# Optimization experiments

Measured on AMD Instinct MI355X. Metric: run time of the kernel, lower is better.

## Reference

```python
import jax, jax.numpy as jnp
import numpy as np

HALF_LOG_2PI = 0.5 * float(np.log(2.0 * np.pi))


def setup_inputs() -> dict:
    key = jax.random.key(0)
    k1, k2 = jax.random.split(key)
    N, D = 16384, 2048
    x = jax.random.normal(k1, (N, D), dtype=jnp.float32)
    raw_params = jax.random.normal(k2, (2 * D,), dtype=jnp.float32)
    # chain spanning tree: edges (i, i+1) for i in 0..D-2  -> shape [D-1, 2]
    idx = jnp.arange(D - 1, dtype=jnp.int64)
    edges = jnp.stack([idx, idx + 1], axis=1)
    return {"x": x, "raw_params": raw_params, "edges": edges}


def reference(x, raw_params, edges):
    # x: [N, D] float; raw_params: [2D] float; edges: [E, 2] int
    D = x.shape[1]
    means = jnp.tanh(raw_params[:D]) * 2.0               # [D]
    stds = jax.nn.softplus(raw_params[D:]) + 1e-6         # [D]
    # Each edge (i, j) contributes logN(x_i) + logN(x_j); equivalently each
    # feature k contributes deg(k) * logN(x_k), deg = endpoint multiplicity.
    deg = jnp.zeros((D,), dtype=x.dtype).at[edges.reshape(-1)].add(1.0)  # [D]
    z = (x - means) / stds                                # [N, D]
    logp = -0.5 * z * z - jnp.log(stds) - HALF_LOG_2PI    # [N, D]
    return logp @ deg                                     # [N]
```

## Files before the change

### kernel.cpp

```cpp
#include <hip/hip_runtime.h>
#include <math.h>

#define HALF_LOG_2PI_F 0.9189385332046727f

typedef float f32x4 __attribute__((ext_vector_type(4)));

__global__ void clt_prep_kernel(const float* __restrict__ rp,
                                const int* __restrict__ edges,
                                float* __restrict__ A,
                                float* __restrict__ B,
                                float* __restrict__ csum,
                                int D, int E) {
    extern __shared__ float sdeg[];
    for (int k = threadIdx.x; k < D; k += blockDim.x) sdeg[k] = 0.0f;
    __syncthreads();
    for (int e = threadIdx.x; e < E; e += blockDim.x) {
        atomicAdd(&sdeg[edges[2 * e]], 1.0f);
        atomicAdd(&sdeg[edges[2 * e + 1]], 1.0f);
    }
    __syncthreads();
    float local_c = 0.0f;
    for (int k = threadIdx.x; k < D; k += blockDim.x) {
        float m = tanhf(rp[k]) * 2.0f;
        float sx = rp[D + k];
        float s = fmaxf(sx, 0.0f) + log1pf(expf(-fabsf(sx))) + 1e-6f;
        float inv_s2 = 1.0f / (s * s);
        float deg = sdeg[k];
        A[k] = deg * (-0.5f * inv_s2);
        B[k] = deg * (m * inv_s2);
        local_c += deg * (-0.5f * m * m * inv_s2 - logf(s) - HALF_LOG_2PI_F);
    }
    __shared__ float wsum[16];
    for (int off = 32; off > 0; off >>= 1)
        local_c += __shfl_down(local_c, off, 64);
    if ((threadIdx.x & 63) == 0) wsum[threadIdx.x >> 6] = local_c;
    __syncthreads();
    if (threadIdx.x == 0) {
        float t = 0.0f;
        int nw = (blockDim.x + 63) >> 6;
        for (int w = 0; w < nw; ++w) t += wsum[w];
        *csum = t;
    }
}

template <int NI>
__global__ __launch_bounds__(256) void clt_slice8nt(
        const float* __restrict__ x,
        const float* __restrict__ A,
        const float* __restrict__ B,
        const float* __restrict__ csum,
        float* __restrict__ out,
        int D) {
    const int lane = threadIdx.x & 63;
    const int w = threadIdx.x >> 6;
    const int colbase = w * (NI * 64);
    const int rowstride = D >> 2;

    const f32x4* Av = (const f32x4*)A;
    const f32x4* Bv = (const f32x4*)B;
    f32x4 a4[NI], b4[NI];
#pragma unroll
    for (int i = 0; i < NI; ++i) {
        a4[i] = Av[colbase + i * 64 + lane];
        b4[i] = Bv[colbase + i * 64 + lane];
    }
    const float c = *csum;

    const int r0 = blockIdx.x * 8;
    const f32x4* xv = (const f32x4*)(x + (size_t)r0 * (size_t)D)
                      + colbase + lane;

    f32x4 xr[8][NI];
#pragma unroll
    for (int r = 0; r < 8; ++r)
#pragma unroll
        for (int i = 0; i < NI; ++i)
            xr[r][i] = __builtin_nontemporal_load(&xv[(size_t)r * rowstride + i * 64]);

    float acc[8];
#pragma unroll
    for (int r = 0; r < 8; ++r) {
        float p = 0.0f, q = 0.0f;
#pragma unroll
        for (int i = 0; i < NI; ++i) {
            f32x4 xq = xr[r][i];
            p += xq.x * fmaf(a4[i].x, xq.x, b4[i].x);
            q += xq.y * fmaf(a4[i].y, xq.y, b4[i].y);
            p += xq.z * fmaf(a4[i].z, xq.z, b4[i].z);
            q += xq.w * fmaf(a4[i].w, xq.w, b4[i].w);
        }
        acc[r] = p + q;
    }

#pragma unroll
    for (int off = 32; off > 0; off >>= 1) {
#pragma unroll
        for (int r = 0; r < 8; ++r)
            acc[r] += __shfl_down(acc[r], off, 64);
    }

    __shared__ float lds[8][4];
    if (lane == 0) {
#pragma unroll
        for (int r = 0; r < 8; ++r) lds[r][w] = acc[r];
    }
    __syncthreads();
    if (threadIdx.x < 8) {
        out[r0 + threadIdx.x] = lds[threadIdx.x][0] + lds[threadIdx.x][1]
                              + lds[threadIdx.x][2] + lds[threadIdx.x][3]
                              + c;
    }
}

__global__ __launch_bounds__(256) void clt_row_generic(
        const float* __restrict__ x,
        const float* __restrict__ A,
        const float* __restrict__ B,
        const float* __restrict__ csum,
        float* __restrict__ out,
        int D) {
    const int row = blockIdx.x;
    float acc = 0.0f;
    for (int k = threadIdx.x; k < D; k += blockDim.x) {
        float xs = x[(size_t)row * (size_t)D + k];
        acc += xs * fmaf(A[k], xs, B[k]);
    }
    for (int off = 32; off > 0; off >>= 1)
        acc += __shfl_down(acc, off, 64);
    __shared__ float wsum[4];
    if ((threadIdx.x & 63) == 0) wsum[threadIdx.x >> 6] = acc;
    __syncthreads();
    if (threadIdx.x == 0)
        out[row] = wsum[0] + wsum[1] + wsum[2] + wsum[3] + *csum;
}

extern "C" void kernel_launch(void* const* d_in, const int* in_sizes, int n_in,
                              void* d_out, int out_size, void* d_ws, size_t ws_size,
                              hipStream_t stream) {
    const float* x     = (const float*)d_in[0];
    const float* rp    = (const float*)d_in[1];
    const int*   edges = (const int*)d_in[2];
    float* out = (float*)d_out;

    const int D = in_sizes[1] / 2;
    const int E = in_sizes[2] / 2;
    const int N = out_size;

    float* A    = (float*)d_ws;
    float* B    = A + D;
    float* csum = B + D;

    clt_prep_kernel<<<1, 1024, D * sizeof(float), stream>>>(rp, edges, A, B, csum, D, E);

    const int NI = D / 1024;
    if (N % 8 == 0 && D == NI * 1024 && (NI == 1 || NI == 2 || NI == 4)) {
        const int nblocks = N / 8;
        switch (NI) {
            case 1:  clt_slice8nt<1><<<nblocks, 256, 0, stream>>>(x, A, B, csum, out, D); break;
            case 2:  clt_slice8nt<2><<<nblocks, 256, 0, stream>>>(x, A, B, csum, out, D); break;
            default: clt_slice8nt<4><<<nblocks, 256, 0, stream>>>(x, A, B, csum, out, D); break;
        }
    } else {
        clt_row_generic<<<N, 256, 0, stream>>>(x, A, B, csum, out, D);
    }
}
```

Measured before the change: 33.62 us.

## Stream x rows into LDS via direct global-to-LDS DMA loads

Replaces the per-thread nontemporal vector register loads of the x tile with __builtin_amdgcn_global_load_lds 16-byte transfers into a per-wave shared buffer. It waits on vmcnt(0) and then reads the values back from LDS for the FMA reduction. The aim is to cut VGPR pressure and issue overhead for the in-flight loads. In exchange it uses 64KB of LDS per block at D=2048, which caps blocks per CU, drops the nontemporal hint, and adds an LDS round trip. The NI=4 specialization is removed, so D=4096 now falls back to the generic kernel.

```diff
diff --git a/kernel.cpp b/kernel.cpp
--- a/kernel.cpp
+++ b/kernel.cpp
@@ -44,7 +44,7 @@
 }
 
 template <int NI>
-__global__ __launch_bounds__(256) void clt_slice8nt(
+__global__ __launch_bounds__(256) void clt_dma(
         const float* __restrict__ x,
         const float* __restrict__ A,
         const float* __restrict__ B,
@@ -54,7 +54,9 @@
     const int lane = threadIdx.x & 63;
     const int w = threadIdx.x >> 6;
     const int colbase = w * (NI * 64);
-    const int rowstride = D >> 2;
+
+    __shared__ float smem[4][8 * NI * 256];
+    __shared__ float lds[8][4];
 
     const f32x4* Av = (const f32x4*)A;
     const f32x4* Bv = (const f32x4*)B;
@@ -67,15 +69,22 @@
     const float c = *csum;
 
     const int r0 = blockIdx.x * 8;
-    const f32x4* xv = (const f32x4*)(x + (size_t)r0 * (size_t)D)
-                      + colbase + lane;
+    const float* gbase = x + (size_t)r0 * (size_t)D;
 
-    f32x4 xr[8][NI];
 #pragma unroll
-    for (int r = 0; r < 8; ++r)
+    for (int r = 0; r < 8; ++r) {
 #pragma unroll
-        for (int i = 0; i < NI; ++i)
-            xr[r][i] = __builtin_nontemporal_load(&xv[(size_t)r * rowstride + i * 64]);
+        for (int i = 0; i < NI; ++i) {
+            const float* g = gbase + (size_t)r * (size_t)D
+                             + ((size_t)(colbase + i * 64 + lane) << 2);
+            __builtin_amdgcn_global_load_lds(
+                (const __attribute__((address_space(1))) unsigned int*)g,
+                (__attribute__((address_space(3))) unsigned int*)
+                    &smem[w][(r * NI + i) * 256],
+                16, 0, 0);
+        }
+    }
+    asm volatile("s_waitcnt vmcnt(0)" ::: "memory");
 
     float acc[8];
 #pragma unroll
@@ -83,7 +92,7 @@
         float p = 0.0f, q = 0.0f;
 #pragma unroll
         for (int i = 0; i < NI; ++i) {
-            f32x4 xq = xr[r][i];
+            f32x4 xq = *(const f32x4*)&smem[w][(r * NI + i) * 256 + lane * 4];
             p += xq.x * fmaf(a4[i].x, xq.x, b4[i].x);
             q += xq.y * fmaf(a4[i].y, xq.y, b4[i].y);
             p += xq.z * fmaf(a4[i].z, xq.z, b4[i].z);
@@ -99,7 +108,6 @@
             acc[r] += __shfl_down(acc[r], off, 64);
     }
 
-    __shared__ float lds[8][4];
     if (lane == 0) {
 #pragma unroll
         for (int r = 0; r < 8; ++r) lds[r][w] = acc[r];
@@ -153,12 +161,11 @@
     clt_prep_kernel<<<1, 1024, D * sizeof(float), stream>>>(rp, edges, A, B, csum, D, E);
 
     const int NI = D / 1024;
-    if (N % 8 == 0 && D == NI * 1024 && (NI == 1 || NI == 2 || NI == 4)) {
+    if (N % 8 == 0 && D == NI * 1024 && (NI == 1 || NI == 2)) {
         const int nblocks = N / 8;
         switch (NI) {
-            case 1:  clt_slice8nt<1><<<nblocks, 256, 0, stream>>>(x, A, B, csum, out, D); break;
-            case 2:  clt_slice8nt<2><<<nblocks, 256, 0, stream>>>(x, A, B, csum, out, D); break;
-            default: clt_slice8nt<4><<<nblocks, 256, 0, stream>>>(x, A, B, csum, out, D); break;
+            case 1:  clt_dma<1><<<nblocks, 256, 0, stream>>>(x, A, B, csum, out, D); break;
+            default: clt_dma<2><<<nblocks, 256, 0, stream>>>(x, A, B, csum, out, D); break;
         }
     } else {
         clt_row_generic<<<N, 256, 0, stream>>>(x, A, B, csum, out, D);
```

Result: slower. 36.80 us (+9.5%).
